# Kernel tuning notes

Hardware: AMD Instinct MI355X
Metric: run time of the kernel (lower is better)

The kernel has to match this reference:

```python
import jax, jax.numpy as jnp
import numpy as np

BOUNDS = 1.6
FEAT = 32
BASE = 128
MULTS = [1, 2, 4]
N = 300000


def setup_inputs() -> dict:
    key = jax.random.key(0)
    ks = jax.random.split(key, 10)
    inp = {"pts": jax.random.normal(ks[0], (N, 3), dtype=jnp.float32)}
    i = 1
    for l, m in enumerate(MULTS):
        R = BASE * m
        for p in range(3):
            inp[f"g{l}{p}"] = jax.random.uniform(ks[i], (FEAT, R, R), minval=0.1, maxval=0.5, dtype=jnp.float32)
            i += 1
    return inp


def bilinear_sample(grid, coords):
    # grid: [C,H,W]; coords: [N,2] in [-1,1], coords[:,0] -> x (W axis), coords[:,1] -> y (H axis)
    # matches F.grid_sample(mode='bilinear', padding_mode='border', align_corners=True)
    C, H, W = grid.shape
    x = jnp.clip((coords[:, 0] + 1.0) * 0.5 * (W - 1), 0.0, W - 1)
    y = jnp.clip((coords[:, 1] + 1.0) * 0.5 * (H - 1), 0.0, H - 1)
    x0 = jnp.floor(x)
    y0 = jnp.floor(y)
    wx = x - x0
    wy = y - y0
    x0i = x0.astype(jnp.int32)
    y0i = y0.astype(jnp.int32)
    x1i = jnp.minimum(x0i + 1, W - 1)
    y1i = jnp.minimum(y0i + 1, H - 1)
    v00 = grid[:, y0i, x0i]  # [C,N]
    v01 = grid[:, y0i, x1i]
    v10 = grid[:, y1i, x0i]
    v11 = grid[:, y1i, x1i]
    out = (v00 * (1.0 - wx) + v01 * wx) * (1.0 - wy) + (v10 * (1.0 - wx) + v11 * wx) * wy
    return out.T  # [N,C]


def reference(pts, g00, g01, g02, g10, g11, g12, g20, g21, g22):
    # normalize_aabb with aabb = [[b,b,b],[-b,-b,-b]] -> (pts-b)*(2/(-2b)) - 1
    p = (pts - BOUNDS) * (2.0 / (-2.0 * BOUNDS)) - 1.0
    # coordinate planes per matMode rows [0,1,1],[1,0,1],[1,1,0]
    planes = [p[:, (1, 2)], p[:, (0, 2)], p[:, (0, 1)]]
    grids = [[g00, g01, g02], [g10, g11, g12], [g20, g21, g22]]
    feats = []
    for level in grids:
        for idx in range(3):
            feats.append(bilinear_sample(level[idx], planes[idx]))
    return jnp.concatenate(feats, axis=-1)  # [N, 3*levels*FEAT]
```

## Files before the change

kernel.cpp:

```cpp
#include <hip/hip_runtime.h>
#include <hip/hip_fp16.h>


typedef float        f32x4 __attribute__((ext_vector_type(4)));
typedef unsigned int u32x4 __attribute__((ext_vector_type(4)));

struct GridPtrs { const float* g[9]; };
struct GridOffs { size_t off[9]; };

#define TP_TEX 64

__global__ __launch_bounds__(256) void transpose_grids_h_kernel(
    GridPtrs gp, GridOffs go, __half* __restrict__ t)
{
    const int b = blockIdx.y;
    const int l = b / 3;
    const int R = 128 << l;
    const int T = R * R;

    const int tile0 = blockIdx.x * TP_TEX;
    if (tile0 >= T) return;

    __shared__ unsigned short lds[TP_TEX * 33];

    const int tid = threadIdx.x;

    {
        const int ch   = tid >> 3;
        const int part = (tid & 7) << 3;
        const float* __restrict__ src = gp.g[b] + (size_t)ch * (size_t)T + tile0 + part;
        const f32x4 a0 = __builtin_nontemporal_load((const f32x4*)src);
        const f32x4 a1 = __builtin_nontemporal_load((const f32x4*)(src + 4));
#pragma unroll
        for (int k = 0; k < 4; ++k)
            lds[(part + k) * 33 + ch] = __half_as_ushort(__float2half_rn(a0[k]));
#pragma unroll
        for (int k = 0; k < 4; ++k)
            lds[(part + 4 + k) * 33 + ch] = __half_as_ushort(__float2half_rn(a1[k]));
    }
    __syncthreads();

    {
        const int tex = tid >> 2;
        const int q   = (tid & 3) << 3;
        const unsigned short* row = &lds[tex * 33 + q];
        u32x4 v;
#pragma unroll
        for (int k = 0; k < 4; ++k) {
            const unsigned lo = row[2 * k];
            const unsigned hi = row[2 * k + 1];
            v[k] = lo | (hi << 16);
        }
        __half* dst = t + go.off[b] + (size_t)(tile0 + tex) * 32 + q;
        *(u32x4*)dst = v;
    }
}

__device__ __forceinline__ void h8_to_f(const uint4 u, float f[8])
{
    const __half2* h = (const __half2*)&u;
#pragma unroll
    for (int i = 0; i < 4; ++i) {
        const float2 t = __half22float2(h[i]);
        f[2 * i + 0] = t.x;
        f[2 * i + 1] = t.y;
    }
}

__global__ __launch_bounds__(256) void triplane_sample_h_kernel(
    const float* __restrict__ pts,
    const __half* __restrict__ tg,
    GridOffs go,
    float* __restrict__ out,
    int n_pts)
{
    const int tid = blockIdx.x * 256 + threadIdx.x;
    const int total = n_pts * 36;
    if (tid >= total) return;

    const int n  = tid / 36;
    const int r  = tid - n * 36;
    const int b  = r >> 2;
    const int ch = (r & 3) << 3;
    const int l  = (b >= 6) ? 2 : (b >= 3 ? 1 : 0);
    const int p  = b - l * 3;

    const float vx = pts[n * 3 + 0];
    const float vy = pts[n * 3 + 1];
    const float vz = pts[n * 3 + 2];

    const float scale = 2.0f / (-2.0f * 1.6f);
    const float px = (vx - 1.6f) * scale - 1.0f;
    const float py = (vy - 1.6f) * scale - 1.0f;
    const float pz = (vz - 1.6f) * scale - 1.0f;

    const float cx = (p == 0) ? py : px;
    const float cy = (p == 2) ? py : pz;

    const int   R   = 128 << l;
    const float Rm1 = (float)(R - 1);

    float x = (cx + 1.0f) * 0.5f * Rm1;
    float y = (cy + 1.0f) * 0.5f * Rm1;
    x = fminf(fmaxf(x, 0.0f), Rm1);
    y = fminf(fmaxf(y, 0.0f), Rm1);

    const float x0f = floorf(x);
    const float y0f = floorf(y);
    const float wx  = x - x0f;
    const float wy  = y - y0f;
    const int x0 = (int)x0f;
    const int y0 = (int)y0f;
    const int x1 = min(x0 + 1, R - 1);
    const int y1 = min(y0 + 1, R - 1);

    const __half* base = tg + go.off[b] + ch;
    const size_t s00 = ((size_t)(y0 * R + x0)) * 32;
    const size_t s01 = ((size_t)(y0 * R + x1)) * 32;
    const size_t s10 = ((size_t)(y1 * R + x0)) * 32;
    const size_t s11 = ((size_t)(y1 * R + x1)) * 32;

    const uint4 u00 = *(const uint4*)(base + s00);
    const uint4 u01 = *(const uint4*)(base + s01);
    const uint4 u10 = *(const uint4*)(base + s10);
    const uint4 u11 = *(const uint4*)(base + s11);

    float f00[8], f01[8], f10[8], f11[8];
    h8_to_f(u00, f00);
    h8_to_f(u01, f01);
    h8_to_f(u10, f10);
    h8_to_f(u11, f11);

    const float omwx = 1.0f - wx;
    const float omwy = 1.0f - wy;

    float res[8];
#pragma unroll
    for (int k = 0; k < 8; ++k) {
        res[k] = (f00[k] * omwx + f01[k] * wx) * omwy
               + (f10[k] * omwx + f11[k] * wx) * wy;
    }

    float* op = out + (size_t)n * 288 + b * 32 + ch;
    const f32x4 r0 = {res[0], res[1], res[2], res[3]};
    const f32x4 r1 = {res[4], res[5], res[6], res[7]};
    __builtin_nontemporal_store(r0, (f32x4*)op);
    __builtin_nontemporal_store(r1, (f32x4*)(op + 4));
}

__global__ __launch_bounds__(256) void triplane_sample_kernel(
    const float* __restrict__ pts,
    GridPtrs gp,
    float* __restrict__ out,
    int n_pts)
{
    const int tid = blockIdx.x * 256 + threadIdx.x;
    const int total = n_pts * 72;
    if (tid >= total) return;

    const int n  = tid / 72;
    const int c4 = tid - n * 72;
    const int b  = c4 >> 3;
    const int ch = (c4 & 7) << 2;
    const int l  = (b >= 6) ? 2 : (b >= 3 ? 1 : 0);
    const int p  = b - l * 3;

    const float vx = pts[n * 3 + 0];
    const float vy = pts[n * 3 + 1];
    const float vz = pts[n * 3 + 2];

    const float scale = 2.0f / (-2.0f * 1.6f);
    const float px = (vx - 1.6f) * scale - 1.0f;
    const float py = (vy - 1.6f) * scale - 1.0f;
    const float pz = (vz - 1.6f) * scale - 1.0f;

    const float cx = (p == 0) ? py : px;
    const float cy = (p == 2) ? py : pz;

    const int   R   = 128 << l;
    const float Rm1 = (float)(R - 1);

    float x = (cx + 1.0f) * 0.5f * Rm1;
    float y = (cy + 1.0f) * 0.5f * Rm1;
    x = fminf(fmaxf(x, 0.0f), Rm1);
    y = fminf(fmaxf(y, 0.0f), Rm1);

    const float x0f = floorf(x);
    const float y0f = floorf(y);
    const float wx  = x - x0f;
    const float wy  = y - y0f;
    const int x0 = (int)x0f;
    const int y0 = (int)y0f;
    const int x1 = min(x0 + 1, R - 1);
    const int y1 = min(y0 + 1, R - 1);

    const size_t RR   = (size_t)R * (size_t)R;
    const float* base = gp.g[b] + (size_t)ch * RR;

    const int i00 = y0 * R + x0;
    const int i01 = y0 * R + x1;
    const int i10 = y1 * R + x0;
    const int i11 = y1 * R + x1;

    const float omwx = 1.0f - wx;
    const float omwy = 1.0f - wy;

    float rr[4];
#pragma unroll
    for (int k = 0; k < 4; ++k) {
        const float* gk = base + (size_t)k * RR;
        rr[k] = (gk[i00] * omwx + gk[i01] * wx) * omwy
              + (gk[i10] * omwx + gk[i11] * wx) * wy;
    }
    ((float4*)out)[tid] = make_float4(rr[0], rr[1], rr[2], rr[3]);
}

extern "C" void kernel_launch(void* const* d_in, const int* in_sizes, int n_in,
                              void* d_out, int out_size, void* d_ws, size_t ws_size,
                              hipStream_t stream)
{
    const float* pts = (const float*)d_in[0];
    GridPtrs gp;
    for (int i = 0; i < 9; ++i) gp.g[i] = (const float*)d_in[1 + i];
    float* out = (float*)d_out;

    const int n_pts = in_sizes[0] / 3;
    const int block = 256;

    GridOffs go;
    size_t off = 0;
    for (int b = 0; b < 9; ++b) {
        go.off[b] = off;
        const int R = 128 << (b / 3);
        off += (size_t)32 * R * R;
    }
    const size_t needed_bytes = off * sizeof(__half);

    if (ws_size >= needed_bytes) {
        __half* tg = (__half*)d_ws;
        dim3 tgrid(4096, 9, 1);
        transpose_grids_h_kernel<<<tgrid, block, 0, stream>>>(gp, go, tg);
        const int total = n_pts * 36;
        const int grid  = (total + block - 1) / block;
        triplane_sample_h_kernel<<<grid, block, 0, stream>>>(pts, tg, go, out, n_pts);
    } else {
        const int total = n_pts * 72;
        const int grid  = (total + block - 1) / block;
        triplane_sample_kernel<<<grid, block, 0, stream>>>(pts, gp, out, n_pts);
    }
}
```

Measured before the change: 551.4 us.

## Duplicate fp16 grids with a one-texel shift so bilinear x-pairs share a line

```diff
diff --git a/kernel.cpp b/kernel.cpp
--- a/kernel.cpp
+++ b/kernel.cpp
@@ -9,6 +9,7 @@
 struct GridOffs { size_t off[9]; };
 
 #define TP_TEX 64
+#define TOTAL_HALVES 33030144ull
 
 __global__ __launch_bounds__(256) void transpose_grids_h_kernel(
     GridPtrs gp, GridOffs go, __half* __restrict__ t)
@@ -51,8 +52,15 @@
             const unsigned hi = row[2 * k + 1];
             v[k] = lo | (hi << 16);
         }
-        __half* dst = t + go.off[b] + (size_t)(tile0 + tex) * 32 + q;
-        *(u32x4*)dst = v;
+        const int g = tile0 + tex;
+        const int x = g & (R - 1);
+
+        __half* A = t + go.off[b];
+        __half* B = t + TOTAL_HALVES + go.off[b];
+
+        *(u32x4*)(A + (size_t)g * 32 + q) = v;
+        if (x >= 1)     *(u32x4*)(B + (size_t)(g - 1) * 32 + q) = v;
+        if (x == R - 1) *(u32x4*)(B + (size_t)g       * 32 + q) = v;
     }
 }
 
@@ -70,7 +78,6 @@
 __global__ __launch_bounds__(256) void triplane_sample_h_kernel(
     const float* __restrict__ pts,
     const __half* __restrict__ tg,
-    GridOffs go,
     float* __restrict__ out,
     int n_pts)
 {
@@ -82,6 +89,89 @@
     const int r  = tid - n * 36;
     const int b  = r >> 2;
     const int ch = (r & 3) << 3;
+    const int l  = (b >= 6) ? 2 : (b >= 3 ? 1 : 0);
+    const int p  = b - l * 3;
+
+    const float vx = pts[n * 3 + 0];
+    const float vy = pts[n * 3 + 1];
+    const float vz = pts[n * 3 + 2];
+
+    const float scale = 2.0f / (-2.0f * 1.6f);
+    const float px = (vx - 1.6f) * scale - 1.0f;
+    const float py = (vy - 1.6f) * scale - 1.0f;
+    const float pz = (vz - 1.6f) * scale - 1.0f;
+
+    const float cx = (p == 0) ? py : px;
+    const float cy = (p == 2) ? py : pz;
+
+    const int   R   = 128 << l;
+    const float Rm1 = (float)(R - 1);
+
+    float x = (cx + 1.0f) * 0.5f * Rm1;
+    float y = (cy + 1.0f) * 0.5f * Rm1;
+    x = fminf(fmaxf(x, 0.0f), Rm1);
+    y = fminf(fmaxf(y, 0.0f), Rm1);
+
+    const float x0f = floorf(x);
+    const float y0f = floorf(y);
+    const float wx  = x - x0f;
+    const float wy  = y - y0f;
+    const int x0 = (int)x0f;
+    const int y0 = (int)y0f;
+    const int y1 = min(y0 + 1, R - 1);
+
+    const int par = x0 & 1;
+    const int xb  = x0 - par;
+
+    const size_t lbase = (l == 0) ? 0ull : ((l == 1) ? 1572864ull : 7864320ull);
+    const size_t off_b = lbase + ((size_t)p << (19 + 2 * l));
+
+    const __half* gbase = tg + (par ? TOTAL_HALVES : 0ull) + off_b + ch;
+    const size_t r0 = ((size_t)(y0 * R + xb)) * 32;
+    const size_t r1 = ((size_t)(y1 * R + xb)) * 32;
+
+    const uint4 u00 = *(const uint4*)(gbase + r0);
+    const uint4 u01 = *(const uint4*)(gbase + r0 + 32);
+    const uint4 u10 = *(const uint4*)(gbase + r1);
+    const uint4 u11 = *(const uint4*)(gbase + r1 + 32);
+
+    float f00[8], f01[8], f10[8], f11[8];
+    h8_to_f(u00, f00);
+    h8_to_f(u01, f01);
+    h8_to_f(u10, f10);
+    h8_to_f(u11, f11);
+
+    const float omwx = 1.0f - wx;
+    const float omwy = 1.0f - wy;
+
+    float res[8];
+#pragma unroll
+    for (int k = 0; k < 8; ++k) {
+        res[k] = (f00[k] * omwx + f01[k] * wx) * omwy
+               + (f10[k] * omwx + f11[k] * wx) * wy;
+    }
+
+    float* op = out + (size_t)n * 288 + b * 32 + ch;
+    const f32x4 r0v = {res[0], res[1], res[2], res[3]};
+    const f32x4 r1v = {res[4], res[5], res[6], res[7]};
+    __builtin_nontemporal_store(r0v, (f32x4*)op);
+    __builtin_nontemporal_store(r1v, (f32x4*)(op + 4));
+}
+
+__global__ __launch_bounds__(256) void triplane_sample_kernel(
+    const float* __restrict__ pts,
+    GridPtrs gp,
+    float* __restrict__ out,
+    int n_pts)
+{
+    const int tid = blockIdx.x * 256 + threadIdx.x;
+    const int total = n_pts * 72;
+    if (tid >= total) return;
+
+    const int n  = tid / 72;
+    const int c4 = tid - n * 72;
+    const int b  = c4 >> 3;
+    const int ch = (c4 & 7) << 2;
     const int l  = (b >= 6) ? 2 : (b >= 3 ? 1 : 0);
     const int p  = b - l * 3;
 
@@ -114,86 +204,6 @@
     const int x1 = min(x0 + 1, R - 1);
     const int y1 = min(y0 + 1, R - 1);
 
-    const __half* base = tg + go.off[b] + ch;
-    const size_t s00 = ((size_t)(y0 * R + x0)) * 32;
-    const size_t s01 = ((size_t)(y0 * R + x1)) * 32;
-    const size_t s10 = ((size_t)(y1 * R + x0)) * 32;
-    const size_t s11 = ((size_t)(y1 * R + x1)) * 32;
-
-    const uint4 u00 = *(const uint4*)(base + s00);
-    const uint4 u01 = *(const uint4*)(base + s01);
-    const uint4 u10 = *(const uint4*)(base + s10);
-    const uint4 u11 = *(const uint4*)(base + s11);
-
-    float f00[8], f01[8], f10[8], f11[8];
-    h8_to_f(u00, f00);
-    h8_to_f(u01, f01);
-    h8_to_f(u10, f10);
-    h8_to_f(u11, f11);
-
-    const float omwx = 1.0f - wx;
-    const float omwy = 1.0f - wy;
-
-    float res[8];
-#pragma unroll
-    for (int k = 0; k < 8; ++k) {
-        res[k] = (f00[k] * omwx + f01[k] * wx) * omwy
-               + (f10[k] * omwx + f11[k] * wx) * wy;
-    }
-
-    float* op = out + (size_t)n * 288 + b * 32 + ch;
-    const f32x4 r0 = {res[0], res[1], res[2], res[3]};
-    const f32x4 r1 = {res[4], res[5], res[6], res[7]};
-    __builtin_nontemporal_store(r0, (f32x4*)op);
-    __builtin_nontemporal_store(r1, (f32x4*)(op + 4));
-}
-
-__global__ __launch_bounds__(256) void triplane_sample_kernel(
-    const float* __restrict__ pts,
-    GridPtrs gp,
-    float* __restrict__ out,
-    int n_pts)
-{
-    const int tid = blockIdx.x * 256 + threadIdx.x;
-    const int total = n_pts * 72;
-    if (tid >= total) return;
-
-    const int n  = tid / 72;
-    const int c4 = tid - n * 72;
-    const int b  = c4 >> 3;
-    const int ch = (c4 & 7) << 2;
-    const int l  = (b >= 6) ? 2 : (b >= 3 ? 1 : 0);
-    const int p  = b - l * 3;
-
-    const float vx = pts[n * 3 + 0];
-    const float vy = pts[n * 3 + 1];
-    const float vz = pts[n * 3 + 2];
-
-    const float scale = 2.0f / (-2.0f * 1.6f);
-    const float px = (vx - 1.6f) * scale - 1.0f;
-    const float py = (vy - 1.6f) * scale - 1.0f;
-    const float pz = (vz - 1.6f) * scale - 1.0f;
-
-    const float cx = (p == 0) ? py : px;
-    const float cy = (p == 2) ? py : pz;
-
-    const int   R   = 128 << l;
-    const float Rm1 = (float)(R - 1);
-
-    float x = (cx + 1.0f) * 0.5f * Rm1;
-    float y = (cy + 1.0f) * 0.5f * Rm1;
-    x = fminf(fmaxf(x, 0.0f), Rm1);
-    y = fminf(fmaxf(y, 0.0f), Rm1);
-
-    const float x0f = floorf(x);
-    const float y0f = floorf(y);
-    const float wx  = x - x0f;
-    const float wy  = y - y0f;
-    const int x0 = (int)x0f;
-    const int y0 = (int)y0f;
-    const int x1 = min(x0 + 1, R - 1);
-    const int y1 = min(y0 + 1, R - 1);
-
     const size_t RR   = (size_t)R * (size_t)R;
     const float* base = gp.g[b] + (size_t)ch * RR;
 
@@ -234,7 +244,7 @@
         const int R = 128 << (b / 3);
         off += (size_t)32 * R * R;
     }
-    const size_t needed_bytes = off * sizeof(__half);
+    const size_t needed_bytes = 2 * off * sizeof(__half);
 
     if (ws_size >= needed_bytes) {
         __half* tg = (__half*)d_ws;
@@ -242,7 +252,7 @@
         transpose_grids_h_kernel<<<tgrid, block, 0, stream>>>(gp, go, tg);
         const int total = n_pts * 36;
         const int grid  = (total + block - 1) / block;
-        triplane_sample_h_kernel<<<grid, block, 0, stream>>>(pts, tg, go, out, n_pts);
+        triplane_sample_h_kernel<<<grid, block, 0, stream>>>(pts, tg, out, n_pts);
     } else {
         const int total = n_pts * 72;
         const int grid  = (total + block - 1) / block;
```

After: 539.0 us, median of 2. 1.02x faster.
